# Performance work log

Hardware: AMD Instinct MI355X
Metric: run time of the kernel (lower is better)

## Reference

```python
import jax, jax.numpy as jnp
import numpy as np

N = 16384      # num nodes
F_IN = 128     # in_features
F_OUT = 128    # out_features


def setup_inputs() -> dict:
    key = jax.random.key(0)
    k1, k2, k3 = jax.random.split(key, 3)
    inp = jax.random.normal(k1, (N, F_IN), dtype=jnp.float32)
    adj = jax.random.uniform(k2, (N, N), dtype=jnp.float32)
    stdv = 1.0 / np.sqrt(F_OUT)
    weight = jax.random.uniform(k3, (F_IN * 2, F_OUT), dtype=jnp.float32,
                                minval=-stdv, maxval=stdv)
    return {"input": inp, "adj": adj, "weight": weight}


def reference(input, adj, weight):
    # support = adj @ input  (dense aggregation, [N, F])
    support = jnp.matmul(adj, input)
    # concat [input, support] -> [N, 2F], then transform -> [N, out]
    # Avoid materializing the concat by splitting the weight matmul:
    w_self, w_agg = weight[:F_IN], weight[F_IN:]
    return jnp.matmul(input, w_self) + jnp.matmul(support, w_agg)
```

## Files before the change

### kernel.cpp

```cpp
#include <hip/hip_runtime.h>


#define NROWS 16384
#define FDIM  128
#define NT2   128

typedef __attribute__((ext_vector_type(4))) float f32x4;
typedef __attribute__((ext_vector_type(8))) short short8;
typedef __attribute__((ext_vector_type(8))) __bf16 bf16x8;
typedef __attribute__((ext_vector_type(4))) unsigned short ushort4v;

static __device__ __forceinline__ unsigned short f2bf(float f) {
  union { __bf16 b; unsigned short u; } cvt;
  cvt.b = (__bf16)f;
  return cvt.u;
}

__global__ __launch_bounds__(256, 2)
void gcn_prep(const float* __restrict__ input, const float* __restrict__ weight,
              unsigned short* __restrict__ Yt, float* __restrict__ Z)
{
  __shared__ __align__(16) unsigned short inA[8192];
  __shared__ __align__(16) unsigned short Wt[32768];
  char* inA_c = (char*)inA;
  char* Wt_c  = (char*)Wt;

  const int tid  = threadIdx.x;
  const int lane = tid & 63;
  const int wv   = tid >> 6;
  const int m0g  = blockIdx.x * 64;

#pragma unroll
  for (int p = 0; p < 8; ++p) {
    const int idx4 = tid + p * 256;
    const int row  = idx4 >> 5;
    const int k0   = (idx4 & 31) * 4;
    const f32x4 v  = *(const f32x4*)(input + (size_t)(m0g + row) * FDIM + k0);
    ushort4v u;
#pragma unroll
    for (int i = 0; i < 4; ++i) u[i] = f2bf(v[i]);
    *(ushort4v*)(inA_c + row * 256 + ((k0 * 2) ^ ((row & 7) << 4))) = u;
  }
#pragma unroll
  for (int p = 0; p < 32; ++p) {
    const int e4   = tid + p * 256;
    const int krow = e4 >> 5;
    const int n0   = (e4 & 31) * 4;
    const f32x4 v  = *(const f32x4*)(weight + (size_t)krow * FDIM + n0);
    const int k  = krow & 127;
    const int nb = (krow >> 7) * 128;
#pragma unroll
    for (int i = 0; i < 4; ++i) {
      const int n = nb + n0 + i;
      *(unsigned short*)(Wt_c + n * 256 + ((k * 2) ^ ((n & 7) << 4))) = f2bf(v[i]);
    }
  }
  __syncthreads();

  const int rlo  = lane & 15;
  const int kgrp = lane >> 4;
  const int arow = wv * 16 + rlo;

  f32x4 acc[16];
#pragma unroll
  for (int f = 0; f < 16; ++f) acc[f] = (f32x4){0.f, 0.f, 0.f, 0.f};

#pragma unroll
  for (int s = 0; s < 4; ++s) {
    const int kb = s * 64 + kgrp * 16;
    const short8 a8 = *(const short8*)(inA_c + arow * 256 + (kb ^ ((arow & 7) << 4)));
#pragma unroll
    for (int f = 0; f < 16; ++f) {
      const int n = f * 16 + rlo;
      const short8 b8 = *(const short8*)(Wt_c + n * 256 + (kb ^ ((n & 7) << 4)));
      acc[f] = __builtin_amdgcn_mfma_f32_16x16x32_bf16(a8, b8, acc[f], 0, 0, 0);
    }
  }

  const int mg = m0g + wv * 16 + kgrp * 4;
#pragma unroll
  for (int f = 0; f < 8; ++f) {
    const int col = f * 16 + rlo;
#pragma unroll
    for (int r = 0; r < 4; ++r)
      Z[(size_t)(mg + r) * FDIM + col] = acc[f][r];
  }
  const int H = mg >> 7, ch = (mg >> 3) & 15, kin0 = mg & 7;
#pragma unroll
  for (int f = 8; f < 16; ++f) {
    const int c = f * 16 + rlo - 128;
    ushort4v u;
#pragma unroll
    for (int r = 0; r < 4; ++r) u[r] = f2bf(acc[f][r]);
    *(ushort4v*)(Yt + (size_t)H * 16384 + (size_t)(ch * 128 + c) * 8 + kin0) = u;
  }
}

__global__ __launch_bounds__(512, 1)
void gcn_main(const float* __restrict__ adj, const unsigned short* __restrict__ Yt,
              const float* __restrict__ Z, float* __restrict__ out)
{
  __shared__ __align__(16) unsigned char lds[2][65536];

  const int tid  = threadIdx.x;
  const int lane = tid & 63;
  const int wv   = tid >> 6;
  const int rg   = wv >> 1;
  const int nh   = wv & 1;
  const int m0   = blockIdx.x * 64;
  const int rlo  = lane & 15;
  const int kgrp = lane >> 4;

  f32x4 acc[4];
#pragma unroll
  for (int f = 0; f < 4; ++f) acc[f] = (f32x4){0.f, 0.f, 0.f, 0.f};

  auto stage = [&](int buf, int kt) {
    const unsigned short* bs = Yt + (size_t)kt * 16384;
#pragma unroll
    for (int i = 0; i < 4; ++i) {
      const int q = wv * 4 + i;
      __builtin_amdgcn_global_load_lds(
          (const __attribute__((address_space(1))) void*)(bs + q * 512 + lane * 8),
          (__attribute__((address_space(3))) void*)(&lds[buf][q * 1024]),
          16, 0, 0);
    }
#pragma unroll
    for (int i = 0; i < 4; ++i) {
      const int p     = wv * 4 + i;
      const int row_g = 2 * p + (lane >> 5);
      const int j     = (lane & 31) ^ (row_g & 7);
      const float* as = adj + (size_t)(m0 + row_g) * NROWS + (size_t)kt * 128 + j * 4;
      __builtin_amdgcn_global_load_lds(
          (const __attribute__((address_space(1))) void*)as,
          (__attribute__((address_space(3))) void*)(&lds[buf][32768 + p * 1024]),
          16, 0, 2 );
    }
  };

  stage(0, 0);
  stage(1, 1);

  const int arow = (rg * 16 + rlo) * 512;
  const int aswz = rlo & 7;

  for (int kt = 0; kt < NT2; ++kt) {
    if (kt < NT2 - 1) {
      asm volatile("s_waitcnt vmcnt(8)" ::: "memory");
    } else {
      asm volatile("s_waitcnt vmcnt(0)" ::: "memory");
    }
    __builtin_amdgcn_sched_barrier(0);
    __builtin_amdgcn_s_barrier();
    __builtin_amdgcn_sched_barrier(0);

    const int buf = kt & 1;
    const unsigned char* Bp = lds[buf];
    const unsigned char* Ap = Bp + 32768;

    short8 a8[4];
#pragma unroll
    for (int s = 0; s < 4; ++s) {
      const int c0 = s * 8 + kgrp * 2;
      const f32x4 lo = *(const f32x4*)(Ap + arow + ((c0    ) ^ aswz) * 16);
      const f32x4 hi = *(const f32x4*)(Ap + arow + ((c0 + 1) ^ aswz) * 16);
      bf16x8 av;
#pragma unroll
      for (int j = 0; j < 4; ++j) {
        av[j]     = (__bf16)lo[j];
        av[j + 4] = (__bf16)hi[j];
      }
      a8[s] = __builtin_bit_cast(short8, av);
    }

#pragma unroll
    for (int s = 0; s < 4; ++s) {
      const int ch = s * 4 + kgrp;
#pragma unroll
      for (int f = 0; f < 4; ++f) {
        const int n = nh * 64 + f * 16 + rlo;
        const short8 b8 = *(const short8*)(Bp + (size_t)(ch * 128 + n) * 16);
        acc[f] = __builtin_amdgcn_mfma_f32_16x16x32_bf16(a8[s], b8, acc[f], 0, 0, 0);
      }
    }

    __builtin_amdgcn_s_barrier();
    __builtin_amdgcn_sched_barrier(0);
    if (kt + 2 < NT2) stage(buf, kt + 2);
  }

  const int rowb = m0 + rg * 16 + (lane >> 4) * 4;
#pragma unroll
  for (int f = 0; f < 4; ++f) {
    const int col = nh * 64 + f * 16 + rlo;
#pragma unroll
    for (int r = 0; r < 4; ++r) {
      const size_t idx = (size_t)(rowb + r) * FDIM + col;
      out[idx] = acc[f][r] + Z[idx];
    }
  }
}

extern "C" void kernel_launch(void* const* d_in, const int* in_sizes, int n_in,
                              void* d_out, int out_size, void* d_ws, size_t ws_size,
                              hipStream_t stream) {
  const float* input  = (const float*)d_in[0];
  const float* adj    = (const float*)d_in[1];
  const float* weight = (const float*)d_in[2];
  float* out = (float*)d_out;

  unsigned short* Yt = (unsigned short*)d_ws;
  float* Z = (float*)((char*)d_ws + (size_t)NROWS * FDIM * 2);

  gcn_prep<<<256, 256, 0, stream>>>(input, weight, Yt, Z);
  gcn_main<<<256, 512, 0, stream>>>(adj, Yt, Z, out);
}
```

Baseline: 198.1 us.

## Convert adj to bf16 once per tile via registers and triple-buffer Yt stages

The main kernel now loads each adj fp32 tile into registers with inline global loads and converts it to bf16 once before writing to LDS. Previously every wave converted fp32 from LDS on each read. The adj K-tile grows to 256 and is split into two compute halves. Yt tiles go through a three-slot rotating LDS buffer with interleaved barriers and vmcnt waits. This aims to cut LDS footprint and bandwidth for A and to overlap adj conversion with MFMA work, at the cost of more registers, complex hand-tuned waitcnt accounting and 160KB of LDS.

Result: slower. 220.3 us (+11.2%).

```diff
diff --git a/kernel.cpp b/kernel.cpp
--- a/kernel.cpp
+++ b/kernel.cpp
@@ -3,7 +3,7 @@
 
 #define NROWS 16384
 #define FDIM  128
-#define NT2   128
+#define NTA   64
 
 typedef __attribute__((ext_vector_type(4))) float f32x4;
 typedef __attribute__((ext_vector_type(8))) short short8;
@@ -96,11 +96,75 @@
   }
 }
 
+
+#define VMCNT(n) do { asm volatile("s_waitcnt vmcnt(" #n ")" ::: "memory");        \
+                      __builtin_amdgcn_sched_barrier(0); } while (0)
+#define LGKM0()  do { asm volatile("s_waitcnt lgkmcnt(0)" ::: "memory");           \
+                      __builtin_amdgcn_sched_barrier(0); } while (0)
+#define BAR()    do { __builtin_amdgcn_s_barrier();                                \
+                      __builtin_amdgcn_sched_barrier(0); } while (0)
+#define SCHED()  __builtin_amdgcn_sched_barrier(0)
+
+#define ALOAD(ka)                                                                  \
+  { const char* _p = abase + (size_t)(ka) * 1024;                                  \
+    asm volatile("global_load_dwordx4 %0, %1, off"            : "=v"(ar[0]) : "v"(_p)); \
+    asm volatile("global_load_dwordx4 %0, %1, off offset:16"  : "=v"(ar[1]) : "v"(_p)); \
+    asm volatile("global_load_dwordx4 %0, %1, off offset:256" : "=v"(ar[2]) : "v"(_p)); \
+    asm volatile("global_load_dwordx4 %0, %1, off offset:272" : "=v"(ar[3]) : "v"(_p)); \
+    asm volatile("global_load_dwordx4 %0, %1, off offset:512" : "=v"(ar[4]) : "v"(_p)); \
+    asm volatile("global_load_dwordx4 %0, %1, off offset:528" : "=v"(ar[5]) : "v"(_p)); \
+    asm volatile("global_load_dwordx4 %0, %1, off offset:768" : "=v"(ar[6]) : "v"(_p)); \
+    asm volatile("global_load_dwordx4 %0, %1, off offset:784" : "=v"(ar[7]) : "v"(_p)); \
+    SCHED(); }
+
+#define ACVT_WRITE(buf)                                                            \
+  { char* _aw = (char*)lds + (size_t)(buf) * 32768 + srow * 512;                   \
+    _Pragma("unroll")                                                              \
+    for (int _j = 0; _j < 4; ++_j) {                                               \
+      bf16x8 _v;                                                                   \
+      _Pragma("unroll")                                                            \
+      for (int _i = 0; _i < 4; ++_i) {                                             \
+        _v[_i]     = (__bf16)ar[2 * _j][_i];                                       \
+        _v[_i + 4] = (__bf16)ar[2 * _j + 1][_i];                                   \
+      }                                                                            \
+      *(short8*)(_aw + (((_j * 8 + sj) ^ (srow & 7)) * 16)) =                      \
+          __builtin_bit_cast(short8, _v);                                          \
+    }                                                                              \
+    SCHED(); }
+
+#define BSTAGE(b, t)                                                               \
+  { const unsigned short* _bs = Yt + (size_t)(t) * 16384;                          \
+    char* _bd = (char*)lds + 65536 + (size_t)(b) * 32768;                          \
+    _Pragma("unroll")                                                              \
+    for (int _i = 0; _i < 4; ++_i) {                                               \
+      const int _q = wv * 4 + _i;                                                  \
+      __builtin_amdgcn_global_load_lds(                                            \
+          (const __attribute__((address_space(1))) void*)(_bs + _q * 512 + lane * 8), \
+          (__attribute__((address_space(3))) void*)(_bd + _q * 1024),              \
+          16, 0, 0);                                                               \
+    }                                                                              \
+    SCHED(); }
+
+#define CHALF(abuf, sub, bbuf)                                                     \
+  { const char* _Ap = (const char*)lds + (size_t)(abuf) * 32768 + arow_b;          \
+    const char* _Bp = (const char*)lds + 65536 + (size_t)(bbuf) * 32768;           \
+    _Pragma("unroll")                                                              \
+    for (int _s = 0; _s < 4; ++_s) {                                               \
+      const int _c = (sub) * 16 + _s * 4 + kgrp;                                   \
+      const short8 _a8 = *(const short8*)(_Ap + ((_c ^ aswz) * 16));               \
+      _Pragma("unroll")                                                            \
+      for (int _f = 0; _f < 4; ++_f) {                                             \
+        const int _n = nh * 64 + _f * 16 + rlo;                                    \
+        const short8 _b8 = *(const short8*)(_Bp + (size_t)((_s * 4 + kgrp) * 128 + _n) * 16); \
+        acc[_f] = __builtin_amdgcn_mfma_f32_16x16x32_bf16(_a8, _b8, acc[_f], 0, 0, 0); \
+      }                                                                            \
+    } }
+
 __global__ __launch_bounds__(512, 1)
 void gcn_main(const float* __restrict__ adj, const unsigned short* __restrict__ Yt,
               const float* __restrict__ Z, float* __restrict__ out)
 {
-  __shared__ __align__(16) unsigned char lds[2][65536];
+  __shared__ __align__(16) unsigned char lds[163840];
 
   const int tid  = threadIdx.x;
   const int lane = tid & 63;
@@ -111,83 +175,66 @@
   const int rlo  = lane & 15;
   const int kgrp = lane >> 4;
 
+  const int srow = tid >> 3;
+  const int sj   = tid & 7;
+  const char* abase = (const char*)(adj + (size_t)(m0 + srow) * NROWS) + sj * 32;
+
+  const int arow_b = (rg * 16 + rlo) * 512;
+  const int aswz   = rlo & 7;
+
   f32x4 acc[4];
 #pragma unroll
   for (int f = 0; f < 4; ++f) acc[f] = (f32x4){0.f, 0.f, 0.f, 0.f};
 
-  auto stage = [&](int buf, int kt) {
-    const unsigned short* bs = Yt + (size_t)kt * 16384;
-#pragma unroll
-    for (int i = 0; i < 4; ++i) {
-      const int q = wv * 4 + i;
-      __builtin_amdgcn_global_load_lds(
-          (const __attribute__((address_space(1))) void*)(bs + q * 512 + lane * 8),
-          (__attribute__((address_space(3))) void*)(&lds[buf][q * 1024]),
-          16, 0, 0);
-    }
-#pragma unroll
-    for (int i = 0; i < 4; ++i) {
-      const int p     = wv * 4 + i;
-      const int row_g = 2 * p + (lane >> 5);
-      const int j     = (lane & 31) ^ (row_g & 7);
-      const float* as = adj + (size_t)(m0 + row_g) * NROWS + (size_t)kt * 128 + j * 4;
-      __builtin_amdgcn_global_load_lds(
-          (const __attribute__((address_space(1))) void*)as,
-          (__attribute__((address_space(3))) void*)(&lds[buf][32768 + p * 1024]),
-          16, 0, 2 );
-    }
-  };
-
-  stage(0, 0);
-  stage(1, 1);
-
-  const int arow = (rg * 16 + rlo) * 512;
-  const int aswz = rlo & 7;
-
-  for (int kt = 0; kt < NT2; ++kt) {
-    if (kt < NT2 - 1) {
-      asm volatile("s_waitcnt vmcnt(8)" ::: "memory");
-    } else {
-      asm volatile("s_waitcnt vmcnt(0)" ::: "memory");
-    }
-    __builtin_amdgcn_sched_barrier(0);
-    __builtin_amdgcn_s_barrier();
-    __builtin_amdgcn_sched_barrier(0);
-
-    const int buf = kt & 1;
-    const unsigned char* Bp = lds[buf];
-    const unsigned char* Ap = Bp + 32768;
-
-    short8 a8[4];
-#pragma unroll
-    for (int s = 0; s < 4; ++s) {
-      const int c0 = s * 8 + kgrp * 2;
-      const f32x4 lo = *(const f32x4*)(Ap + arow + ((c0    ) ^ aswz) * 16);
-      const f32x4 hi = *(const f32x4*)(Ap + arow + ((c0 + 1) ^ aswz) * 16);
-      bf16x8 av;
-#pragma unroll
-      for (int j = 0; j < 4; ++j) {
-        av[j]     = (__bf16)lo[j];
-        av[j + 4] = (__bf16)hi[j];
-      }
-      a8[s] = __builtin_bit_cast(short8, av);
-    }
-
-#pragma unroll
-    for (int s = 0; s < 4; ++s) {
-      const int ch = s * 4 + kgrp;
-#pragma unroll
-      for (int f = 0; f < 4; ++f) {
-        const int n = nh * 64 + f * 16 + rlo;
-        const short8 b8 = *(const short8*)(Bp + (size_t)(ch * 128 + n) * 16);
-        acc[f] = __builtin_amdgcn_mfma_f32_16x16x32_bf16(a8[s], b8, acc[f], 0, 0, 0);
-      }
-    }
-
-    __builtin_amdgcn_s_barrier();
-    __builtin_amdgcn_sched_barrier(0);
-    if (kt + 2 < NT2) stage(buf, kt + 2);
-  }
+  f32x4 ar[8];
+
+  ALOAD(0);
+  BSTAGE(0, 0);
+  BSTAGE(1, 1);
+  VMCNT(8);
+  ACVT_WRITE(0);
+  ALOAD(1);
+  VMCNT(12);
+  LGKM0();
+  BAR();
+
+  BSTAGE(2, 2);
+  CHALF(0, 0, 0);
+  VMCNT(12);
+  BAR();
+  BSTAGE(0, 3);
+  CHALF(0, 1, 1);
+  VMCNT(8);
+  ACVT_WRITE(1);
+  VMCNT(4);
+  LGKM0();
+  BAR();
+
+  int bA = 2;
+  for (int kt = 1; kt <= NTA - 2; ++kt) {
+    const int abufC = kt & 1;
+    const int bS0   = bA >= 1 ? bA - 1 : bA + 2;
+    const int bS1   = bA;
+    const int bC1   = bA < 2 ? bA + 1 : 0;
+    ALOAD(kt + 1);
+    BSTAGE(bS0, 2 * kt + 2);
+    CHALF(abufC, 0, bA);
+    VMCNT(12);
+    BAR();
+    BSTAGE(bS1, 2 * kt + 3);
+    CHALF(abufC, 1, bC1);
+    VMCNT(8);
+    ACVT_WRITE(abufC ^ 1);
+    VMCNT(4);
+    LGKM0();
+    BAR();
+    bA = bS0;
+  }
+
+  CHALF(1, 0, 0);
+  VMCNT(0);
+  BAR();
+  CHALF(1, 1, 1);
 
   const int rowb = m0 + rg * 16 + (lane >> 4) * 4;
 #pragma unroll
```

## Fold self-term matmul into main K loop as an extra tile

Applied to the files above, without the earlier changes.

The input@W_self term is no longer computed in the prep kernel and written to a float Z buffer. Instead W_self is transposed to bf16 and stored as a 129th K-tile of Yt, and the main kernel runs one extra iteration that loads the input rows in place of adj. This removes the Z write and read and shrinks the prep kernel. In exchange the self term now accumulates through bf16 inputs rather than being kept in fp32.

After: 187.9 us. 1.05x faster.

```diff
diff --git a/kernel.cpp b/kernel.cpp
--- a/kernel.cpp
+++ b/kernel.cpp
@@ -3,7 +3,7 @@
 
 #define NROWS 16384
 #define FDIM  128
-#define NT2   128
+#define NT3   129
 
 typedef __attribute__((ext_vector_type(4))) float f32x4;
 typedef __attribute__((ext_vector_type(8))) short short8;
@@ -18,10 +18,10 @@
 
 __global__ __launch_bounds__(256, 2)
 void gcn_prep(const float* __restrict__ input, const float* __restrict__ weight,
-              unsigned short* __restrict__ Yt, float* __restrict__ Z)
+              unsigned short* __restrict__ Yt)
 {
   __shared__ __align__(16) unsigned short inA[8192];
-  __shared__ __align__(16) unsigned short Wt[32768];
+  __shared__ __align__(16) unsigned short Wt[16384];
   char* inA_c = (char*)inA;
   char* Wt_c  = (char*)Wt;
 
@@ -29,6 +29,13 @@
   const int lane = tid & 63;
   const int wv   = tid >> 6;
   const int m0g  = blockIdx.x * 64;
+
+  if (tid < 64) {
+    const int e = blockIdx.x * 64 + tid;
+    const int k = e >> 7, n = e & 127;
+    Yt[(size_t)128 * 16384 + (size_t)((k >> 3) * 128 + n) * 8 + (k & 7)] =
+        f2bf(weight[(size_t)k * FDIM + n]);
+  }
 
 #pragma unroll
   for (int p = 0; p < 8; ++p) {
@@ -42,16 +49,15 @@
     *(ushort4v*)(inA_c + row * 256 + ((k0 * 2) ^ ((row & 7) << 4))) = u;
   }
 #pragma unroll
-  for (int p = 0; p < 32; ++p) {
+  for (int p = 0; p < 16; ++p) {
     const int e4   = tid + p * 256;
-    const int krow = e4 >> 5;
+    const int krow = 128 + (e4 >> 5);
     const int n0   = (e4 & 31) * 4;
     const f32x4 v  = *(const f32x4*)(weight + (size_t)krow * FDIM + n0);
-    const int k  = krow & 127;
-    const int nb = (krow >> 7) * 128;
-#pragma unroll
-    for (int i = 0; i < 4; ++i) {
-      const int n = nb + n0 + i;
+    const int k = krow & 127;
+#pragma unroll
+    for (int i = 0; i < 4; ++i) {
+      const int n = n0 + i;
       *(unsigned short*)(Wt_c + n * 256 + ((k * 2) ^ ((n & 7) << 4))) = f2bf(v[i]);
     }
   }
@@ -61,16 +67,16 @@
   const int kgrp = lane >> 4;
   const int arow = wv * 16 + rlo;
 
-  f32x4 acc[16];
-#pragma unroll
-  for (int f = 0; f < 16; ++f) acc[f] = (f32x4){0.f, 0.f, 0.f, 0.f};
+  f32x4 acc[8];
+#pragma unroll
+  for (int f = 0; f < 8; ++f) acc[f] = (f32x4){0.f, 0.f, 0.f, 0.f};
 
 #pragma unroll
   for (int s = 0; s < 4; ++s) {
     const int kb = s * 64 + kgrp * 16;
     const short8 a8 = *(const short8*)(inA_c + arow * 256 + (kb ^ ((arow & 7) << 4)));
 #pragma unroll
-    for (int f = 0; f < 16; ++f) {
+    for (int f = 0; f < 8; ++f) {
       const int n = f * 16 + rlo;
       const short8 b8 = *(const short8*)(Wt_c + n * 256 + (kb ^ ((n & 7) << 4)));
       acc[f] = __builtin_amdgcn_mfma_f32_16x16x32_bf16(a8, b8, acc[f], 0, 0, 0);
@@ -78,17 +84,10 @@
   }
 
   const int mg = m0g + wv * 16 + kgrp * 4;
+  const int H = mg >> 7, ch = (mg >> 3) & 15, kin0 = mg & 7;
 #pragma unroll
   for (int f = 0; f < 8; ++f) {
-    const int col = f * 16 + rlo;
-#pragma unroll
-    for (int r = 0; r < 4; ++r)
-      Z[(size_t)(mg + r) * FDIM + col] = acc[f][r];
-  }
-  const int H = mg >> 7, ch = (mg >> 3) & 15, kin0 = mg & 7;
-#pragma unroll
-  for (int f = 8; f < 16; ++f) {
-    const int c = f * 16 + rlo - 128;
+    const int c = f * 16 + rlo;
     ushort4v u;
 #pragma unroll
     for (int r = 0; r < 4; ++r) u[r] = f2bf(acc[f][r]);
@@ -97,8 +96,8 @@
 }
 
 __global__ __launch_bounds__(512, 1)
-void gcn_main(const float* __restrict__ adj, const unsigned short* __restrict__ Yt,
-              const float* __restrict__ Z, float* __restrict__ out)
+void gcn_main(const float* __restrict__ adj, const float* __restrict__ input,
+              const unsigned short* __restrict__ Yt, float* __restrict__ out)
 {
   __shared__ __align__(16) unsigned char lds[2][65536];
 
@@ -115,7 +114,7 @@
 #pragma unroll
   for (int f = 0; f < 4; ++f) acc[f] = (f32x4){0.f, 0.f, 0.f, 0.f};
 
-  auto stage = [&](int buf, int kt) {
+  auto stageB = [&](int buf, int kt) {
     const unsigned short* bs = Yt + (size_t)kt * 16384;
 #pragma unroll
     for (int i = 0; i < 4; ++i) {
@@ -125,6 +124,8 @@
           (__attribute__((address_space(3))) void*)(&lds[buf][q * 1024]),
           16, 0, 0);
     }
+  };
+  auto stageA = [&](int buf, int kt) {
 #pragma unroll
     for (int i = 0; i < 4; ++i) {
       const int p     = wv * 4 + i;
@@ -137,15 +138,29 @@
           16, 0, 2 );
     }
   };
-
-  stage(0, 0);
-  stage(1, 1);
+  auto stageF = [&](int buf) {
+    stageB(buf, 128);
+#pragma unroll
+    for (int i = 0; i < 4; ++i) {
+      const int p     = wv * 4 + i;
+      const int row_g = 2 * p + (lane >> 5);
+      const int j     = (lane & 31) ^ (row_g & 7);
+      const float* as = input + (size_t)(m0 + row_g) * FDIM + j * 4;
+      __builtin_amdgcn_global_load_lds(
+          (const __attribute__((address_space(1))) void*)as,
+          (__attribute__((address_space(3))) void*)(&lds[buf][32768 + p * 1024]),
+          16, 0, 0);
+    }
+  };
+
+  stageB(0, 0); stageA(0, 0);
+  stageB(1, 1); stageA(1, 1);
 
   const int arow = (rg * 16 + rlo) * 512;
   const int aswz = rlo & 7;
 
-  for (int kt = 0; kt < NT2; ++kt) {
-    if (kt < NT2 - 1) {
+  for (int kt = 0; kt < NT3; ++kt) {
+    if (kt < NT3 - 1) {
       asm volatile("s_waitcnt vmcnt(8)" ::: "memory");
     } else {
       asm volatile("s_waitcnt vmcnt(0)" ::: "memory");
@@ -186,7 +201,10 @@
 
     __builtin_amdgcn_s_barrier();
     __builtin_amdgcn_sched_barrier(0);
-    if (kt + 2 < NT2) stage(buf, kt + 2);
+    if (kt + 2 < NT3) {
+      if (kt + 2 == 128) stageF(buf);
+      else { stageB(buf, kt + 2); stageA(buf, kt + 2); }
+    }
   }
 
   const int rowb = m0 + rg * 16 + (lane >> 4) * 4;
@@ -196,7 +214,7 @@
 #pragma unroll
     for (int r = 0; r < 4; ++r) {
       const size_t idx = (size_t)(rowb + r) * FDIM + col;
-      out[idx] = acc[f][r] + Z[idx];
+      out[idx] = acc[f][r];
     }
   }
 }
@@ -210,8 +228,7 @@
   float* out = (float*)d_out;
 
   unsigned short* Yt = (unsigned short*)d_ws;
-  float* Z = (float*)((char*)d_ws + (size_t)NROWS * FDIM * 2);
-
-  gcn_prep<<<256, 256, 0, stream>>>(input, weight, Yt, Z);
-  gcn_main<<<256, 512, 0, stream>>>(adj, Yt, Z, out);
-}
+
+  gcn_prep<<<256, 256, 0, stream>>>(input, weight, Yt);
+  gcn_main<<<256, 512, 0, stream>>>(adj, input, Yt, out);
+}
```
